# Performance work log

Hardware: AMD Instinct MI355X
Metric: run time of the kernel (lower is better)

Reference implementation:

```python
import jax, jax.numpy as jnp
import numpy as np

D_MODEL = 1024
N_HEADS = 16
D_HEAD = D_MODEL // N_HEADS


def setup_inputs() -> dict:
    key = jax.random.key(0)
    ks = jax.random.split(key, 9)
    B, S = 2, 2048
    s = 0.02
    return {
        "x": jax.random.normal(ks[0], (B, S, D_MODEL), dtype=jnp.float32),
        "Wq": jax.random.normal(ks[1], (D_MODEL, D_MODEL), dtype=jnp.float32) * s,
        "bq": jnp.zeros((D_MODEL,), dtype=jnp.float32),
        "Wk": jax.random.normal(ks[2], (D_MODEL, D_MODEL), dtype=jnp.float32) * s,
        "bk": jnp.zeros((D_MODEL,), dtype=jnp.float32),
        "Wv": jax.random.normal(ks[3], (D_MODEL, D_MODEL), dtype=jnp.float32) * s,
        "bv": jnp.zeros((D_MODEL,), dtype=jnp.float32),
        "Wo": jax.random.normal(ks[4], (D_MODEL, D_MODEL), dtype=jnp.float32) * s,
        "bo": jnp.zeros((D_MODEL,), dtype=jnp.float32),
    }


def reference(x, Wq, bq, Wk, bk, Wv, bv, Wo, bo):
    B, S, _ = x.shape
    # projections -> [B, H, S, Dh]
    def split_heads(t):
        return t.reshape(B, S, N_HEADS, D_HEAD).transpose(0, 2, 1, 3)
    Q = split_heads(x @ Wq + bq)
    K = split_heads(x @ Wk + bk)
    V = split_heads(x @ Wv + bv)
    scores = jnp.einsum('bhqd,bhkd->bhqk', Q, K)  # [B,H,S,S]
    mask = jnp.tril(jnp.ones((S, S), dtype=bool))
    # NB: original masks BEFORE scaling (mask fill -1e9 then /sqrt(d_head))
    scores = jnp.where(mask[None, None], scores, jnp.float32(-1e9))
    scores = scores / jnp.sqrt(jnp.float32(D_HEAD))
    attn = jax.nn.softmax(scores, axis=-1)
    ctx = jnp.einsum('bhqk,bhkd->bhqd', attn, V)
    ctx = ctx.transpose(0, 2, 1, 3).reshape(B, S, D_MODEL)
    return ctx @ Wo + bo
```

## Files before the change

kernel.cpp:

```cpp
#include <hip/hip_runtime.h>

typedef __bf16 bf16;
typedef __bf16 bf16x8 __attribute__((ext_vector_type(8)));
typedef __bf16 bf16x4 __attribute__((ext_vector_type(4)));
typedef float  f32x4  __attribute__((ext_vector_type(4)));

#define D_MODEL 1024
#define S_LEN   2048
#define NHEAD   16
#define DHEAD   64
#define BATCH   2
#define MROWS   (BATCH * S_LEN)

#define QSCALE 0.18033688011112042f

__device__ __forceinline__ void gld_lds16(const void* g, void* lds_base) {
    __builtin_amdgcn_global_load_lds(
        (const __attribute__((address_space(1))) void*)g,
        (__attribute__((address_space(3))) void*)lds_base, 16, 0, 0);
}

__global__ void prep_kernel(const float* __restrict__ x,
                            const float* __restrict__ W0, const float* __restrict__ W1,
                            const float* __restrict__ W2, const float* __restrict__ W3,
                            bf16* __restrict__ xb, bf16* __restrict__ Wt) {
    int tx = threadIdx.x, ty = threadIdx.y;
    if (blockIdx.z == 4) {
        int tid = ty * 32 + tx;
        size_t base = ((size_t)blockIdx.y * 32 + blockIdx.x) * 4096;
#pragma unroll
        for (int j = 0; j < 4; j++) {
            size_t i = base + (size_t)(j * 256 + tid) * 4;
            f32x4 v = *(const f32x4*)(x + i);
            bf16x4 o;
            o[0] = (bf16)v[0]; o[1] = (bf16)v[1]; o[2] = (bf16)v[2]; o[3] = (bf16)v[3];
            *(bf16x4*)(xb + i) = o;
        }
        return;
    }
    __shared__ float tile[32][33];
    const float* W = (blockIdx.z == 0) ? W0 : (blockIdx.z == 1) ? W1
                   : (blockIdx.z == 2) ? W2 : W3;
    int n0 = blockIdx.x * 32, k0 = blockIdx.y * 32;
#pragma unroll
    for (int j = 0; j < 4; j++)
        tile[ty + 8 * j][tx] = W[(size_t)(k0 + ty + 8 * j) * D_MODEL + n0 + tx];
    __syncthreads();
    bf16* out = Wt + (size_t)blockIdx.z * D_MODEL * D_MODEL;
#pragma unroll
    for (int j = 0; j < 4; j++)
        out[(size_t)(n0 + ty + 8 * j) * D_MODEL + k0 + tx] = (bf16)tile[tx][ty + 8 * j];
}

__global__ __launch_bounds__(512, 2) void gemm0_kernel(
    const bf16* __restrict__ A, const bf16* __restrict__ Bt,
    const float* __restrict__ b0, const float* __restrict__ b1, const float* __restrict__ b2,
    bf16* __restrict__ Qo, bf16* __restrict__ Ko, bf16* __restrict__ Vto) {
    __shared__ bf16 sA[2][2][128 * 64];
    __shared__ bf16 sB[2][2][128 * 64];
    const int t = threadIdx.x;
    const int wave = t >> 6, lane = t & 63;
    const int quad = lane >> 4, m16 = lane & 15;
    const int wm = wave >> 2, wn = wave & 3;
    const int s7 = m16 & 7;
    const int p   = blockIdx.x;
    const int r8  = p & 7;
    const int idx = p >> 3;
    const int xl  = idx % 6, yl = idx / 6;
    const int xb2 = (r8 & 1) * 6 + xl;
    const int yb2 = (r8 >> 1) * 4 + yl;
    const int row0 = yb2 * 256, col0 = xb2 * 256;
    constexpr int NKT = D_MODEL / 64;

    f32x4 acc[8][4];
#pragma unroll
    for (int i = 0; i < 8; i++)
#pragma unroll
        for (int j = 0; j < 4; j++) acc[i][j] = (f32x4){0.f, 0.f, 0.f, 0.f};

    auto stageA = [&](int T, int slot, int h) {
#pragma unroll
        for (int i = 0; i < 2; i++) {
            int cb = i * 512 + wave * 64;
            int c  = cb + lane;
            int r  = c >> 3, sl = c & 7;
            int gk = sl ^ (r & 7);
            gld_lds16(A + (size_t)(row0 + h * 128 + r) * D_MODEL + T * 64 + gk * 8,
                      (char*)&sA[slot][h][0] + cb * 16);
        }
    };
    auto stageB = [&](int T, int slot, int h) {
#pragma unroll
        for (int i = 0; i < 2; i++) {
            int cb = i * 512 + wave * 64;
            int c  = cb + lane;
            int r  = c >> 3, sl = c & 7;
            int gk = sl ^ (r & 7);
            gld_lds16(Bt + (size_t)(col0 + h * 128 + r) * D_MODEL + T * 64 + gk * 8,
                      (char*)&sB[slot][h][0] + cb * 16);
        }
    };

    stageA(0, 0, 0); stageB(0, 0, 0);
    stageA(0, 0, 1); stageB(0, 0, 1);
    stageA(1, 1, 0); stageB(1, 1, 0);
    asm volatile("s_waitcnt vmcnt(4)" ::: "memory");
    asm volatile("s_barrier" ::: "memory");

    for (int T = 0; T < NKT; ++T) {
        const int s = T & 1;
#pragma unroll
        for (int q = 0; q < 4; ++q) {
            const int qa = q >> 1, qb = q & 1;
            const bf16* Ah = &sA[s][qa][0];
            const bf16* Bh = &sB[s][qb][0];
            bf16x8 af[4][2], bfr[2][2];
#pragma unroll
            for (int mi = 0; mi < 4; mi++)
#pragma unroll
                for (int kst = 0; kst < 2; kst++)
                    af[mi][kst] = *(const bf16x8*)
                        &Ah[(wm * 64 + mi * 16 + m16) * 64
                            + (((kst * 4 + quad) ^ s7) * 8)];
#pragma unroll
            for (int ni = 0; ni < 2; ni++)
#pragma unroll
                for (int kst = 0; kst < 2; kst++)
                    bfr[ni][kst] = *(const bf16x8*)
                        &Bh[(wn * 32 + ni * 16 + m16) * 64
                            + (((kst * 4 + quad) ^ s7) * 8)];
            if (q == 0)      { if (T + 1 < NKT) stageA(T + 1, s ^ 1, 1); }
            else if (q == 1) { if (T + 1 < NKT) stageB(T + 1, s ^ 1, 1); }
            else if (q == 2) { if (T + 2 < NKT) stageA(T + 2, s, 0); }
            else             { if (T + 2 < NKT) stageB(T + 2, s, 0); }
            asm volatile("s_barrier" ::: "memory");
            __builtin_amdgcn_s_setprio(1);
#pragma unroll
            for (int kst = 0; kst < 2; kst++)
#pragma unroll
                for (int mi = 0; mi < 4; mi++)
#pragma unroll
                    for (int ni = 0; ni < 2; ni++)
                        acc[qa * 4 + mi][qb * 2 + ni] =
                            __builtin_amdgcn_mfma_f32_16x16x32_bf16(
                                af[mi][kst], bfr[ni][kst],
                                acc[qa * 4 + mi][qb * 2 + ni], 0, 0, 0);
            __builtin_amdgcn_s_setprio(0);
            if (q == 3) {
                if (T < NKT - 2)
                    asm volatile("s_waitcnt vmcnt(4)" ::: "memory");
                else if (T == NKT - 2)
                    asm volatile("s_waitcnt vmcnt(0)" ::: "memory");
            }
            asm volatile("s_barrier" ::: "memory");
        }
    }

    int sel = col0 >> 10;
    const float* bias_arr = (sel == 0) ? b0 : (sel == 1) ? b1 : b2;
#pragma unroll
    for (int a = 0; a < 8; a++) {
        int ha = a >> 2, mi = a & 3;
        int s0g = row0 + ha * 128 + wm * 64 + mi * 16 + quad * 4;
        int b = s0g >> 11, ss0 = s0g & 2047;
#pragma unroll
        for (int c2 = 0; c2 < 4; c2++) {
            int hb = c2 >> 1, ni = c2 & 1;
            int col = col0 + hb * 128 + wn * 32 + ni * 16 + m16;
            int cn = col & 1023;
            int h = cn >> 6, d = cn & 63;
            float bias = bias_arr[cn];
            if (sel < 2) {
                bf16* dst = (sel == 0) ? Qo : Ko;
                float scl = (sel == 0) ? QSCALE : 1.0f;
                size_t base = (((size_t)b * NHEAD + h) * S_LEN);
#pragma unroll
                for (int r = 0; r < 4; r++)
                    dst[(base + ss0 + r) * DHEAD + d] =
                        (bf16)((acc[a][c2][r] + bias) * scl);
            } else {
                bf16x4 pk;
#pragma unroll
                for (int r = 0; r < 4; r++) pk[r] = (bf16)(acc[a][c2][r] + bias);
                *(bf16x4*)(Vto + (((size_t)b * NHEAD + h) * DHEAD + d) * S_LEN + ss0) = pk;
            }
        }
    }
}

__global__ __launch_bounds__(512, 4) void gemm1_kernel(
    const bf16* __restrict__ A, const bf16* __restrict__ Bt,
    const float* __restrict__ bias, float* __restrict__ Co) {
    __shared__ bf16 sA[3][2][128 * 32];
    __shared__ bf16 sB[3][2][64 * 32];
    const int t = threadIdx.x;
    const int wave = t >> 6, lane = t & 63;
    const int quad = lane >> 4, m16 = lane & 15;
    const int grp = wave >> 2, w4 = wave & 3;
    const int wrow = w4 * 32;
    const int p  = blockIdx.x;
    const int xb = (p >> 3) & 15;
    const int yb = (p & 7) + 8 * (p >> 7);
    const int row0 = yb * 128, col0 = xb * 64;
    const int kbase = grp * 512;
    constexpr int NK = 16;

    f32x4 acc[2][4];
#pragma unroll
    for (int i = 0; i < 2; i++)
#pragma unroll
        for (int j = 0; j < 4; j++) acc[i][j] = (f32x4){0.f, 0.f, 0.f, 0.f};

    auto stage = [&](int kk, int buf) {
#pragma unroll
        for (int i = 0; i < 2; i++) {
            int cb = i * 256 + w4 * 64;
            int c  = cb + lane;
            int r  = c >> 2, kg = c & 3;
            int gk = kg ^ ((r >> 1) & 3);
            gld_lds16(A + (size_t)(row0 + r) * D_MODEL + kbase + kk * 32 + gk * 8,
                      (char*)&sA[buf][grp][0] + cb * 16);
        }
        {
            int cb = w4 * 64;
            int c  = cb + lane;
            int r  = c >> 2, kg = c & 3;
            int gk = kg ^ ((r >> 1) & 3);
            gld_lds16(Bt + (size_t)(col0 + r) * D_MODEL + kbase + kk * 32 + gk * 8,
                      (char*)&sB[buf][grp][0] + cb * 16);
        }
    };

    stage(0, 0);
    stage(1, 1);

    const int sx = (m16 >> 1) & 3;
    for (int ks = 0; ks < NK; ++ks) {
        if (ks + 1 < NK)
            asm volatile("s_waitcnt vmcnt(3)\n\ts_barrier" ::: "memory");
        else
            asm volatile("s_waitcnt vmcnt(0)\n\ts_barrier" ::: "memory");
        if (ks + 2 < NK) stage(ks + 2, (ks + 2) % 3);

        const int cur = ks % 3;
        const int gg = (quad ^ sx) * 8;
        bf16x8 af[2], bfr[4];
#pragma unroll
        for (int mi = 0; mi < 2; mi++)
            af[mi] = *(const bf16x8*)&sA[cur][grp][(wrow + mi * 16 + m16) * 32 + gg];
#pragma unroll
        for (int ni = 0; ni < 4; ni++)
            bfr[ni] = *(const bf16x8*)&sB[cur][grp][(ni * 16 + m16) * 32 + gg];
#pragma unroll
        for (int mi = 0; mi < 2; mi++)
#pragma unroll
            for (int ni = 0; ni < 4; ni++)
                acc[mi][ni] = __builtin_amdgcn_mfma_f32_16x16x32_bf16(
                    af[mi], bfr[ni], acc[mi][ni], 0, 0, 0);
    }

    __syncthreads();
    float* scr = (float*)&sA[0][0][0];
    if (grp == 1) {
#pragma unroll
        for (int mi = 0; mi < 2; mi++)
#pragma unroll
            for (int ni = 0; ni < 4; ni++)
#pragma unroll
                for (int r = 0; r < 4; r++)
                    scr[(wrow + mi * 16 + quad * 4 + r) * 66 + ni * 16 + m16] =
                        acc[mi][ni][r];
    }
    __syncthreads();
    if (grp == 0) {
#pragma unroll
        for (int mi = 0; mi < 2; mi++)
#pragma unroll
            for (int ni = 0; ni < 4; ni++) {
                int col = col0 + ni * 16 + m16;
                float bb = bias[col];
#pragma unroll
                for (int r = 0; r < 4; r++) {
                    int row = wrow + mi * 16 + quad * 4 + r;
                    Co[(size_t)(row0 + row) * D_MODEL + col] =
                        acc[mi][ni][r] + scr[row * 66 + ni * 16 + m16] + bb;
                }
            }
    }
}

__global__ __launch_bounds__(256, 4) void attn_kernel(
    const bf16* __restrict__ Q, const bf16* __restrict__ K,
    const bf16* __restrict__ Vt, bf16* __restrict__ ctx) {
    __shared__ bf16 Kt_s[2][64 * 64];
    __shared__ bf16 Vt_s[2][64 * 64];

    const int t = threadIdx.x, wave = t >> 6, lane = t & 63;
    const int quad = lane >> 4, m16 = lane & 15;
    const int bh = blockIdx.x;
    const int qt = 31 - blockIdx.y;
    const int nt = qt + 1;
    const size_t base = (size_t)bh * S_LEN * DHEAD;

    bf16x8 aq[2];
#pragma unroll
    for (int kst = 0; kst < 2; kst++)
        aq[kst] = *(const bf16x8*)(Q + base
            + (size_t)(qt * 64 + wave * 16 + m16) * DHEAD + kst * 32 + quad * 8);

    f32x4 o[4];
#pragma unroll
    for (int di = 0; di < 4; di++) o[di] = (f32x4){0.f, 0.f, 0.f, 0.f};
    float l_acc = 0.f;

    auto stage = [&](int j, int buf) {
#pragma unroll
        for (int i = 0; i < 2; i++) {
            int cb = i * 256 + wave * 64;
            int c  = cb + lane;
            int pos = c >> 3, g = c & 7;
            int gk = g ^ (pos & 7);
            gld_lds16(K  + base + (size_t)(j * 64 + pos) * DHEAD + gk * 8,
                      (char*)&Kt_s[buf][0] + cb * 16);
            gld_lds16(Vt + base + (size_t)pos * S_LEN + j * 64 + gk * 8,
                      (char*)&Vt_s[buf][0] + cb * 16);
        }
    };

    stage(0, 0);

    for (int j = 0; j < nt; ++j) {
        asm volatile("s_waitcnt vmcnt(0)\n\ts_barrier" ::: "memory");
        if (j + 1 < nt) stage(j + 1, (j + 1) & 1);

        const int cur = j & 1;
        const int kt0 = j * 64;

        f32x4 sc[4];
#pragma unroll
        for (int ni = 0; ni < 4; ni++) sc[ni] = (f32x4){0.f, 0.f, 0.f, 0.f};
        __builtin_amdgcn_s_setprio(1);
#pragma unroll
        for (int ni = 0; ni < 4; ni++) {
            int pos = ni * 16 + m16;
#pragma unroll
            for (int kst = 0; kst < 2; kst++) {
                int gg = (kst * 4 + quad) ^ (pos & 7);
                bf16x8 kf = *(const bf16x8*)&Kt_s[cur][pos * 64 + gg * 8];
                sc[ni] = __builtin_amdgcn_mfma_f32_16x16x32_bf16(
                    kf, aq[kst], sc[ni], 0, 0, 0);
            }
        }
        __builtin_amdgcn_s_setprio(0);

        if (j == qt) {
            int qg = qt * 64 + wave * 16 + m16;
#pragma unroll
            for (int ni = 0; ni < 4; ni++)
#pragma unroll
                for (int r = 0; r < 4; r++) {
                    int kp = kt0 + ni * 16 + quad * 4 + r;
                    if (kp > qg) sc[ni][r] = -1e9f;
                }
        }

        unsigned int pd[4][2];
        {
            float ls0 = 0.f, ls1 = 0.f;
#pragma unroll
            for (int ni = 0; ni < 4; ni++) {
                float p0 = __builtin_amdgcn_exp2f(sc[ni][0]);
                float p1 = __builtin_amdgcn_exp2f(sc[ni][1]);
                float p2 = __builtin_amdgcn_exp2f(sc[ni][2]);
                float p3 = __builtin_amdgcn_exp2f(sc[ni][3]);
                union { bf16x4 h; unsigned int u[2]; } cv;
                cv.h[0] = (bf16)p0; cv.h[1] = (bf16)p1;
                cv.h[2] = (bf16)p2; cv.h[3] = (bf16)p3;
                pd[ni][0] = cv.u[0];
                pd[ni][1] = cv.u[1];
                ls0 += p0 + p1;
                ls1 += p2 + p3;
            }
            l_acc += ls0 + ls1;
        }

#pragma unroll
        for (int kst = 0; kst < 2; kst++) {
            unsigned int x0 = pd[2 * kst][0],     y0 = pd[2 * kst][1];
            unsigned int x1 = pd[2 * kst + 1][0], y1 = pd[2 * kst + 1][1];
            asm("v_permlane32_swap_b32 %0, %1" : "+v"(x0), "+v"(x1));
            asm("v_permlane32_swap_b32 %0, %1" : "+v"(y0), "+v"(y1));
            asm("v_permlane16_swap_b32 %0, %1" : "+v"(x0), "+v"(x1));
            asm("v_permlane16_swap_b32 %0, %1" : "+v"(y0), "+v"(y1));
            union { unsigned int u[4]; bf16x8 v; } pk;
            pk.u[0] = x0; pk.u[1] = y0; pk.u[2] = x1; pk.u[3] = y1;
            bf16x8 ap = pk.v;
            __builtin_amdgcn_s_setprio(1);
#pragma unroll
            for (int di = 0; di < 4; di++) {
                int d = di * 16 + m16;
                int gg = (kst * 4 + quad) ^ (d & 7);
                bf16x8 vf = *(const bf16x8*)&Vt_s[cur][d * 64 + gg * 8];
                o[di] = __builtin_amdgcn_mfma_f32_16x16x32_bf16(
                    vf, ap, o[di], 0, 0, 0);
            }
            __builtin_amdgcn_s_setprio(0);
        }
    }

    int b = bh >> 4, h = bh & 15;
    float l = l_acc;
    l += __shfl_xor(l, 16);
    l += __shfl_xor(l, 32);
    float rl = 1.0f / l;
    int s = qt * 64 + wave * 16 + m16;
#pragma unroll
    for (int di = 0; di < 4; di++) {
        bf16x4 pk;
#pragma unroll
        for (int r = 0; r < 4; r++) pk[r] = (bf16)(o[di][r] * rl);
        *(bf16x4*)(ctx + ((size_t)b * S_LEN + s) * D_MODEL
                   + h * DHEAD + di * 16 + quad * 4) = pk;
    }
}

extern "C" void kernel_launch(void* const* d_in, const int* in_sizes, int n_in,
                              void* d_out, int out_size, void* d_ws, size_t ws_size,
                              hipStream_t stream) {
    const float* x  = (const float*)d_in[0];
    const float* Wq = (const float*)d_in[1];
    const float* bq = (const float*)d_in[2];
    const float* Wk = (const float*)d_in[3];
    const float* bk = (const float*)d_in[4];
    const float* Wv = (const float*)d_in[5];
    const float* bv = (const float*)d_in[6];
    const float* Wo = (const float*)d_in[7];
    const float* bo = (const float*)d_in[8];
    float* out = (float*)d_out;

    char* ws = (char*)d_ws;
    const size_t MB = 1u << 20;
    bf16* xb  = (bf16*)(ws + 0);
    bf16* Wt  = (bf16*)(ws + 8  * MB);
    bf16* Qb  = (bf16*)(ws + 16 * MB);
    bf16* Kb  = (bf16*)(ws + 24 * MB);
    bf16* Vtb = (bf16*)(ws + 32 * MB);
    bf16* ctx = (bf16*)(ws + 0);

    prep_kernel<<<dim3(32, 32, 5), dim3(32, 8), 0, stream>>>(x, Wq, Wk, Wv, Wo,
                                                             xb, Wt);
    gemm0_kernel<<<dim3(192), 512, 0, stream>>>(xb, Wt, bq, bk, bv,
                                                Qb, Kb, Vtb);
    attn_kernel<<<dim3(32, 32), 256, 0, stream>>>(Qb, Kb, Vtb, ctx);
    gemm1_kernel<<<dim3(512), 512, 0, stream>>>(ctx, Wt + 3 * 1024 * 1024,
                                                bo, out);
}
```

Measured before the change: 188.0 us.

## Reorder GEMM quadrant traversal in a snake pattern to reuse A/B fragments

Restructures the projection GEMM main loop so the four 128x128 quadrants are visited in a serpentine order (A0B0, A0B1, A1B1, A1B0). Each step reuses the register fragments from the previous step, so only one of A or B is reread from LDS per quadrant, which cuts LDS read traffic. The global-to-LDS staging schedule and the vmcnt waits are reworked to match, with waits now issued twice per K-tile. The tighter wait and barrier choreography risks stalls or races if the counts are wrong.

```diff
diff --git a/kernel.cpp b/kernel.cpp
--- a/kernel.cpp
+++ b/kernel.cpp
@@ -101,60 +101,78 @@
         }
     };
 
+#define RD_A(AF, AH)                                                        \
+    _Pragma("unroll") for (int mi = 0; mi < 4; mi++)                        \
+    _Pragma("unroll") for (int kst = 0; kst < 2; kst++)                     \
+        AF[mi][kst] = *(const bf16x8*)                                      \
+            &(AH)[(wm * 64 + mi * 16 + m16) * 64 + (((kst * 4 + quad) ^ s7) * 8)];
+#define RD_B(BF, BH)                                                        \
+    _Pragma("unroll") for (int ni = 0; ni < 2; ni++)                        \
+    _Pragma("unroll") for (int kst = 0; kst < 2; kst++)                     \
+        BF[ni][kst] = *(const bf16x8*)                                      \
+            &(BH)[(wn * 32 + ni * 16 + m16) * 64 + (((kst * 4 + quad) ^ s7) * 8)];
+#define MMQ(AM, BN)                                                         \
+    _Pragma("unroll") for (int kst = 0; kst < 2; kst++)                     \
+    _Pragma("unroll") for (int mi = 0; mi < 4; mi++)                        \
+    _Pragma("unroll") for (int ni = 0; ni < 2; ni++)                        \
+        acc[(AM) + mi][(BN) + ni] = __builtin_amdgcn_mfma_f32_16x16x32_bf16(\
+            af[mi][kst], bfr[ni][kst], acc[(AM) + mi][(BN) + ni], 0, 0, 0);
+#define BAR() asm volatile("s_barrier" ::: "memory")
+
     stageA(0, 0, 0); stageB(0, 0, 0);
     stageA(0, 0, 1); stageB(0, 0, 1);
-    stageA(1, 1, 0); stageB(1, 1, 0);
-    asm volatile("s_waitcnt vmcnt(4)" ::: "memory");
-    asm volatile("s_barrier" ::: "memory");
+    stageA(1, 1, 0);
+    asm volatile("s_waitcnt vmcnt(2)" ::: "memory");
+    BAR();
 
     for (int T = 0; T < NKT; ++T) {
         const int s = T & 1;
-#pragma unroll
-        for (int q = 0; q < 4; ++q) {
-            const int qa = q >> 1, qb = q & 1;
-            const bf16* Ah = &sA[s][qa][0];
-            const bf16* Bh = &sB[s][qb][0];
-            bf16x8 af[4][2], bfr[2][2];
-#pragma unroll
-            for (int mi = 0; mi < 4; mi++)
-#pragma unroll
-                for (int kst = 0; kst < 2; kst++)
-                    af[mi][kst] = *(const bf16x8*)
-                        &Ah[(wm * 64 + mi * 16 + m16) * 64
-                            + (((kst * 4 + quad) ^ s7) * 8)];
-#pragma unroll
-            for (int ni = 0; ni < 2; ni++)
-#pragma unroll
-                for (int kst = 0; kst < 2; kst++)
-                    bfr[ni][kst] = *(const bf16x8*)
-                        &Bh[(wn * 32 + ni * 16 + m16) * 64
-                            + (((kst * 4 + quad) ^ s7) * 8)];
-            if (q == 0)      { if (T + 1 < NKT) stageA(T + 1, s ^ 1, 1); }
-            else if (q == 1) { if (T + 1 < NKT) stageB(T + 1, s ^ 1, 1); }
-            else if (q == 2) { if (T + 2 < NKT) stageA(T + 2, s, 0); }
-            else             { if (T + 2 < NKT) stageB(T + 2, s, 0); }
-            asm volatile("s_barrier" ::: "memory");
-            __builtin_amdgcn_s_setprio(1);
-#pragma unroll
-            for (int kst = 0; kst < 2; kst++)
-#pragma unroll
-                for (int mi = 0; mi < 4; mi++)
-#pragma unroll
-                    for (int ni = 0; ni < 2; ni++)
-                        acc[qa * 4 + mi][qb * 2 + ni] =
-                            __builtin_amdgcn_mfma_f32_16x16x32_bf16(
-                                af[mi][kst], bfr[ni][kst],
-                                acc[qa * 4 + mi][qb * 2 + ni], 0, 0, 0);
-            __builtin_amdgcn_s_setprio(0);
-            if (q == 3) {
-                if (T < NKT - 2)
-                    asm volatile("s_waitcnt vmcnt(4)" ::: "memory");
-                else if (T == NKT - 2)
-                    asm volatile("s_waitcnt vmcnt(0)" ::: "memory");
-            }
-            asm volatile("s_barrier" ::: "memory");
-        }
-    }
+        const bf16* A0h = &sA[s][0][0];
+        const bf16* A1h = &sA[s][1][0];
+        const bf16* B0h = &sB[s][0][0];
+        const bf16* B1h = &sB[s][1][0];
+        bf16x8 af[4][2], bfr[2][2];
+
+        RD_A(af, A0h); RD_B(bfr, B0h);
+        if (T + 1 < NKT) stageB(T + 1, s ^ 1, 1);
+        BAR();
+        __builtin_amdgcn_s_setprio(1);
+        MMQ(0, 0);
+        __builtin_amdgcn_s_setprio(0);
+        BAR();
+
+        RD_B(bfr, B1h);
+        if (T + 1 < NKT) stageB(T + 1, s ^ 1, 0);
+        BAR();
+        __builtin_amdgcn_s_setprio(1);
+        MMQ(0, 2);
+        __builtin_amdgcn_s_setprio(0);
+        if (T < NKT - 2) asm volatile("s_waitcnt vmcnt(4)" ::: "memory");
+        else             asm volatile("s_waitcnt vmcnt(0)" ::: "memory");
+        BAR();
+
+        RD_A(af, A1h);
+        if (T + 2 < NKT) stageA(T + 2, s, 0);
+        BAR();
+        __builtin_amdgcn_s_setprio(1);
+        MMQ(4, 2);
+        __builtin_amdgcn_s_setprio(0);
+        BAR();
+
+        RD_B(bfr, B0h);
+        if (T + 1 < NKT) stageA(T + 1, s ^ 1, 1);
+        BAR();
+        __builtin_amdgcn_s_setprio(1);
+        MMQ(4, 0);
+        __builtin_amdgcn_s_setprio(0);
+        if (T < NKT - 2) asm volatile("s_waitcnt vmcnt(4)" ::: "memory");
+        else             asm volatile("s_waitcnt vmcnt(0)" ::: "memory");
+        BAR();
+    }
+#undef RD_A
+#undef RD_B
+#undef MMQ
+#undef BAR
 
     int sel = col0 >> 10;
     const float* bias_arr = (sel == 0) ? b0 : (sel == 1) ? b1 : b2;
```

Result: faster. 175.2 us (-6.8%).
